# Kernel tuning notes

Measured on AMD Instinct MI355X. Metric: run time of the kernel, lower is better.

## Reference

```python
import jax, jax.numpy as jnp
import numpy as np

N = 100000       # nodes
E = 1200000      # edges (before self loops)
IN = 3
H = 64           # hidden
HNUM = 256       # number of direct virtual nodes
L = 2            # layers - 1 (hidden GATConvs and VN MLPs)
NEG_SLOPE = 0.2  # GATConv default


def setup_inputs() -> dict:
    key = jax.random.key(0)
    ks = jax.random.split(key, 20)
    s_in = 1.0 / np.sqrt(IN)
    s_h = 1.0 / np.sqrt(H)
    inp = dict(
        x=jax.random.normal(ks[0], (N, IN), dtype=jnp.float32),
        edge_index=jax.random.randint(ks[1], (2, E), 0, N, dtype=jnp.int32),
        h_blocks=jax.random.randint(ks[2], (N,), 0, HNUM, dtype=jnp.int32),
        h_levels=jax.random.randint(ks[3], (N,), 0, 4, dtype=jnp.int32),
        h_num=HNUM,
        # initial GATConv(IN -> H)
        w_in=jax.random.normal(ks[4], (IN, H), dtype=jnp.float32) * s_in,
        a_src_in=jax.random.normal(ks[5], (H,), dtype=jnp.float32) * s_h,
        a_dst_in=jax.random.normal(ks[6], (H,), dtype=jnp.float32) * s_h,
        b_in=jnp.zeros((H,), dtype=jnp.float32),
        # L hidden GATConv(H -> H) layers, stacked
        w_l=jax.random.normal(ks[7], (L, H, H), dtype=jnp.float32) * s_h,
        a_src_l=jax.random.normal(ks[8], (L, H), dtype=jnp.float32) * s_h,
        a_dst_l=jax.random.normal(ks[9], (L, H), dtype=jnp.float32) * s_h,
        b_l=jnp.zeros((L, H), dtype=jnp.float32),
        # L virtual-node MLPs: Linear-ReLU-Linear-ReLU
        mlp_w1=jax.random.normal(ks[10], (L, H, H), dtype=jnp.float32) * s_h,
        mlp_b1=jnp.zeros((L, H), dtype=jnp.float32),
        mlp_w2=jax.random.normal(ks[11], (L, H, H), dtype=jnp.float32) * s_h,
        mlp_b2=jnp.zeros((L, H), dtype=jnp.float32),
        # virtualnode embedding, constant-initialized to 0 in original
        vn_emb=jnp.zeros((1, H), dtype=jnp.float32),
    )
    return inp


def _gat_conv(x, src, dst, n, W, a_src, a_dst, b):
    """PyG GATConv, heads=1, add_self_loops already in (src,dst)."""
    h = x @ W                                   # [n, H]
    alpha = jax.nn.leaky_relu((h @ a_src)[src] + (h @ a_dst)[dst], NEG_SLOPE)
    # softmax over incoming edges of each dst node (self-loops => nonempty)
    amax = jax.ops.segment_max(alpha, dst, num_segments=n)
    ex = jnp.exp(alpha - amax[dst])
    denom = jax.ops.segment_sum(ex, dst, num_segments=n)
    w = ex / denom[dst]                         # [E_total]
    out = jax.ops.segment_sum(w[:, None] * h[src], dst, num_segments=n)
    return out + b


def _mlp(v, w1, b1, w2, b2):
    return jax.nn.relu(jax.nn.relu(v @ w1 + b1) @ w2 + b2)


def reference(x, edge_index, h_blocks, h_levels, h_num,
              w_in, a_src_in, a_dst_in, b_in,
              w_l, a_src_l, a_dst_l, b_l,
              mlp_w1, mlp_b1, mlp_w2, mlp_b2, vn_emb):
    n = x.shape[0]
    loops = jnp.arange(n, dtype=edge_index.dtype)
    src = jnp.concatenate([edge_index[0], loops])
    dst = jnp.concatenate([edge_index[1], loops])

    out = _gat_conv(x, src, dst, n, w_in, a_src_in, a_dst_in, b_in)
    vn_direct = jnp.broadcast_to(vn_emb, (h_num, vn_emb.shape[1]))  # zeros init
    vn_root = vn_emb                                                # [1, H]

    for l in range(L):
        out = out + vn_direct[h_blocks]
        out = _gat_conv(out, src, dst, n, w_l[l], a_src_l[l], a_dst_l[l], b_l[l])
        vn_direct = jax.ops.segment_sum(out, h_blocks, num_segments=h_num) + vn_direct
        vn_direct = vn_direct + vn_root
        vn_root = jnp.sum(vn_direct, axis=0, keepdims=True) + vn_root
        # original applies ALL vn MLPs each layer (faithful reproduction)
        for m in range(L):
            vn_direct = _mlp(vn_direct, mlp_w1[m], mlp_b1[m], mlp_w2[m], mlp_b2[m])
            vn_root = _mlp(vn_root, mlp_w1[m], mlp_b1[m], mlp_w2[m], mlp_b2[m])
    return out
```

## Files before the change

### kernel.cpp

```cpp
#include <hip/hip_runtime.h>


typedef __attribute__((ext_vector_type(8))) short short8;
typedef __attribute__((ext_vector_type(4))) float f32x4;

__device__ __forceinline__ unsigned short f2bf(float x){
    unsigned u = __float_as_uint(x);
    unsigned r = (u + 0x7fffu + ((u >> 16) & 1u)) >> 16;
    return (unsigned short)r;
}
__device__ __forceinline__ float bf2f(unsigned short b){
    return __uint_as_float(((unsigned)b) << 16);
}

#define BSHIFT 9
#define CHUNK 4096
#define NSLICE 8

__device__ __forceinline__ int incl_scan256(int v, int* sums4){
    int lane = threadIdx.x & 63, w = threadIdx.x >> 6;
    int x = v;
    #pragma unroll
    for (int o = 1; o < 64; o <<= 1){ int t = __shfl_up(x, o, 64); if (lane >= o) x += t; }
    __syncthreads();
    if (lane == 63) sums4[w] = x;
    __syncthreads();
    for (int j = 0; j < w; ++j) x += sums4[j];
    return x;
}

__global__ __launch_bounds__(256) void k_count(const int* __restrict__ dst, int E, int NB,
                                               int* __restrict__ bucketCount,
                                               const int* __restrict__ hb, int N,
                                               int* __restrict__ hbBins){
    __shared__ int cnt[256], cnt2[256];
    cnt[threadIdx.x] = 0; cnt2[threadIdx.x] = 0;
    __syncthreads();
    int base = blockIdx.x*CHUNK;
    int lim = min(base + CHUNK, E);
    for (int i = base + threadIdx.x; i < lim; i += 256)
        atomicAdd(&cnt[dst[i] >> BSHIFT], 1);
    int limN = min(base + CHUNK, N);
    for (int i = base + threadIdx.x; i < limN; i += 256)
        atomicAdd(&cnt2[hb[i]], 1);
    __syncthreads();
    if (threadIdx.x < NB && cnt[threadIdx.x])
        atomicAdd(&bucketCount[threadIdx.x], cnt[threadIdx.x]);
    if (cnt2[threadIdx.x])
        atomicAdd(&hbBins[threadIdx.x], cnt2[threadIdx.x]);
}

__global__ __launch_bounds__(256) void k_scan_all(const int* __restrict__ bucketCount,
                                                  int NB, int E, int N,
                                                  int* __restrict__ bucketOff,
                                                  int* __restrict__ bucketCur,
                                                  int* __restrict__ rowptr,
                                                  const int* __restrict__ hbBins,
                                                  int* __restrict__ binptr,
                                                  int* __restrict__ bincur){
    __shared__ int sums4[4];
    int tid = threadIdx.x;
    int v = (tid < NB) ? bucketCount[tid] : 0;
    int x = incl_scan256(v, sums4);
    if (tid < NB){ bucketOff[tid] = x - v; bucketCur[tid] = x - v; }
    if (tid == NB-1) bucketOff[NB] = x;
    if (tid == 0) rowptr[N] = E;
    int v2 = hbBins[tid];
    int x2 = incl_scan256(v2, sums4);
    binptr[tid] = x2 - v2;
    bincur[tid] = x2 - v2;
    if (tid == 255) binptr[256] = x2;
}

__global__ __launch_bounds__(256) void k_bucket_place(const int* __restrict__ src,
                                                      const int* __restrict__ dst, int E, int NB,
                                                      int* __restrict__ bucketCur,
                                                      int2* __restrict__ pairs){
    __shared__ int cnt[256], binStart[256], binCur[256], chunkBase[256];
    __shared__ int sums4[4];
    __shared__ int2 lp[CHUNK];
    int tid = threadIdx.x;
    cnt[tid] = 0; binCur[tid] = 0;
    __syncthreads();
    int base = blockIdx.x*CHUNK;
    int s[16], d[16];
    #pragma unroll
    for (int k = 0; k < 16; ++k){
        int i = base + k*256 + tid;
        if (i < E){ s[k] = src[i]; d[k] = dst[i]; atomicAdd(&cnt[d[k] >> BSHIFT], 1); }
        else d[k] = -1;
    }
    __syncthreads();
    int v = cnt[tid];
    int x = incl_scan256(v, sums4);
    binStart[tid] = x - v;
    __syncthreads();
    #pragma unroll
    for (int k = 0; k < 16; ++k){
        if (d[k] >= 0){
            int b = d[k] >> BSHIFT;
            int p = binStart[b] + atomicAdd(&binCur[b], 1);
            lp[p] = make_int2(s[k], d[k]);
        }
    }
    if (tid < NB){
        int c = cnt[tid];
        chunkBase[tid] = c ? atomicAdd(&bucketCur[tid], c) : 0;
    }
    __syncthreads();
    int total = min(CHUNK, E - base);
    for (int i = tid; i < total; i += 256){
        int2 p = lp[i];
        int b = p.y >> BSHIFT;
        pairs[chunkBase[b] + (i - binStart[b])] = p;
    }
}

__global__ __launch_bounds__(256) void k_hb_place(const int* __restrict__ hb, int N,
                                                  int* __restrict__ bincur,
                                                  int* __restrict__ nodes){
    __shared__ int cnt[256], binStart[256], binCur[256], chunkBase[256];
    __shared__ int sums4[4];
    __shared__ int lp[CHUNK];
    __shared__ unsigned char lb[CHUNK];
    int tid = threadIdx.x;
    cnt[tid] = 0; binCur[tid] = 0;
    __syncthreads();
    int base = blockIdx.x*CHUNK;
    int key[16];
    #pragma unroll
    for (int k = 0; k < 16; ++k){
        int i = base + k*256 + tid;
        key[k] = (i < N) ? hb[i] : -1;
        if (key[k] >= 0) atomicAdd(&cnt[key[k]], 1);
    }
    __syncthreads();
    int v = cnt[tid];
    int x = incl_scan256(v, sums4);
    binStart[tid] = x - v;
    __syncthreads();
    #pragma unroll
    for (int k = 0; k < 16; ++k){
        if (key[k] >= 0){
            int p = binStart[key[k]] + atomicAdd(&binCur[key[k]], 1);
            lp[p] = base + k*256 + tid;
            lb[p] = (unsigned char)key[k];
        }
    }
    if (cnt[tid]) chunkBase[tid] = atomicAdd(&bincur[tid], cnt[tid]);
    __syncthreads();
    int total = min(CHUNK, N - base);
    for (int i = tid; i < total; i += 256){
        int b = lb[i];
        nodes[chunkBase[b] + (i - binStart[b])] = lp[i];
    }
}

__global__ __launch_bounds__(256) void k_bucket_csr(const int2* __restrict__ pairs,
                                                    const int* __restrict__ bucketOff, int N,
                                                    int* __restrict__ rowptr,
                                                    int* __restrict__ colarr){
    __shared__ int deg[512], cur[512];
    __shared__ int sums4[4];
    __shared__ int tAs;
    int b = blockIdx.x, tid = threadIdx.x;
    int d0 = b << BSHIFT;
    int e0 = bucketOff[b], e1 = bucketOff[b+1];
    deg[tid] = 0; deg[256+tid] = 0;
    __syncthreads();
    for (int i = e0 + tid; i < e1; i += 256)
        atomicAdd(&deg[pairs[i].y - d0], 1);
    __syncthreads();
    int vA = deg[tid], vB = deg[256+tid];
    int xA = incl_scan256(vA, sums4);
    if (tid == 255) tAs = xA;
    int xB = incl_scan256(vB, sums4) + tAs;
    int exclA = xA - vA, exclB = xB - vB;
    cur[tid] = exclA; cur[256+tid] = exclB;
    int dA = d0 + tid, dB = d0 + 256 + tid;
    if (dA < N) rowptr[dA] = e0 + exclA;
    if (dB < N) rowptr[dB] = e0 + exclB;
    __syncthreads();
    for (int i = e0 + tid; i < e1; i += 256){
        int2 p = pairs[i];
        int pos = e0 + atomicAdd(&cur[p.y - d0], 1);
        colarr[pos] = p.x;
    }
}

__global__ __launch_bounds__(256) void k_transform_in(const float* __restrict__ x,
                                                      const float* __restrict__ W,
                                                      const float* __restrict__ a_src,
                                                      const float* __restrict__ a_dst,
                                                      unsigned short* __restrict__ hout,
                                                      float* __restrict__ ssrc,
                                                      float* __restrict__ sdst, int N){
    int wv = blockIdx.x*4 + (threadIdx.x >> 6);
    int lane = threadIdx.x & 63;
    if (wv >= N) return;
    float acc = 0.f;
    #pragma unroll
    for (int k = 0; k < 3; ++k)
        acc += x[wv*3 + k] * W[k*64 + lane];
    hout[(size_t)wv*64 + lane] = f2bf(acc);
    float v1 = acc * a_src[lane];
    float v2 = acc * a_dst[lane];
    #pragma unroll
    for (int o = 32; o; o >>= 1){ v1 += __shfl_xor(v1, o, 64); v2 += __shfl_xor(v2, o, 64); }
    if (lane == 0){ ssrc[wv] = v1; sdst[wv] = v2; }
}

#define LDW 72
__global__ __launch_bounds__(256) void k_transform_h_mfma(const float* __restrict__ feat,
                                                          const float* __restrict__ vn,
                                                          const float* __restrict__ vn_emb,
                                                          const int* __restrict__ hb,
                                                          const float* __restrict__ W,
                                                          const float* __restrict__ a_src,
                                                          const float* __restrict__ a_dst,
                                                          unsigned short* __restrict__ hout,
                                                          float* __restrict__ ssrc,
                                                          float* __restrict__ sdst, int N){
    __shared__ unsigned short WhT[64*LDW], WlT[64*LDW], Ah[64*LDW], Al[64*LDW];
    const int n0 = blockIdx.x * 64;

    for (int idx = threadIdx.x; idx < 4096; idx += 256){
        int n = idx >> 6, k = idx & 63;
        float w = W[k*64 + n];
        unsigned short hi = f2bf(w);
        WhT[n*LDW + k] = hi;
        WlT[n*LDW + k] = f2bf(w - bf2f(hi));
    }
    for (int t = threadIdx.x; t < 1024; t += 256){
        int row = t >> 4, c4 = t & 15;
        int node = n0 + row;
        float4 v = make_float4(0.f,0.f,0.f,0.f);
        if (node < N){
            v = ((const float4*)feat)[(size_t)node*16 + c4];
            float4 g = vn ? ((const float4*)vn)[(size_t)hb[node]*16 + c4]
                          : ((const float4*)vn_emb)[c4];
            v.x += g.x; v.y += g.y; v.z += g.z; v.w += g.w;
        }
        int base = row*LDW + c4*4;
        unsigned short h0 = f2bf(v.x), h1 = f2bf(v.y), h2 = f2bf(v.z), h3 = f2bf(v.w);
        Ah[base+0] = h0; Al[base+0] = f2bf(v.x - bf2f(h0));
        Ah[base+1] = h1; Al[base+1] = f2bf(v.y - bf2f(h1));
        Ah[base+2] = h2; Al[base+2] = f2bf(v.z - bf2f(h2));
        Ah[base+3] = h3; Al[base+3] = f2bf(v.w - bf2f(h3));
    }
    __syncthreads();

    int lane = threadIdx.x & 63;
    int wv   = threadIdx.x >> 6;
    int mrow = lane & 15, quad = lane >> 4;
    int m0 = wv * 16;

    f32x4 acc0 = {0,0,0,0}, acc1 = {0,0,0,0}, acc2 = {0,0,0,0}, acc3 = {0,0,0,0};
    #pragma unroll
    for (int k0 = 0; k0 < 64; k0 += 32){
        int kb = k0 + quad*8;
        short8 ah = *(const short8*)&Ah[(m0+mrow)*LDW + kb];
        short8 al = *(const short8*)&Al[(m0+mrow)*LDW + kb];
        short8 b0h = *(const short8*)&WhT[( 0+mrow)*LDW + kb];
        short8 b1h = *(const short8*)&WhT[(16+mrow)*LDW + kb];
        short8 b2h = *(const short8*)&WhT[(32+mrow)*LDW + kb];
        short8 b3h = *(const short8*)&WhT[(48+mrow)*LDW + kb];
        short8 b0l = *(const short8*)&WlT[( 0+mrow)*LDW + kb];
        short8 b1l = *(const short8*)&WlT[(16+mrow)*LDW + kb];
        short8 b2l = *(const short8*)&WlT[(32+mrow)*LDW + kb];
        short8 b3l = *(const short8*)&WlT[(48+mrow)*LDW + kb];
        acc0 = __builtin_amdgcn_mfma_f32_16x16x32_bf16(ah, b0h, acc0, 0, 0, 0);
        acc1 = __builtin_amdgcn_mfma_f32_16x16x32_bf16(ah, b1h, acc1, 0, 0, 0);
        acc2 = __builtin_amdgcn_mfma_f32_16x16x32_bf16(ah, b2h, acc2, 0, 0, 0);
        acc3 = __builtin_amdgcn_mfma_f32_16x16x32_bf16(ah, b3h, acc3, 0, 0, 0);
        acc0 = __builtin_amdgcn_mfma_f32_16x16x32_bf16(ah, b0l, acc0, 0, 0, 0);
        acc1 = __builtin_amdgcn_mfma_f32_16x16x32_bf16(ah, b1l, acc1, 0, 0, 0);
        acc2 = __builtin_amdgcn_mfma_f32_16x16x32_bf16(ah, b2l, acc2, 0, 0, 0);
        acc3 = __builtin_amdgcn_mfma_f32_16x16x32_bf16(ah, b3l, acc3, 0, 0, 0);
        acc0 = __builtin_amdgcn_mfma_f32_16x16x32_bf16(al, b0h, acc0, 0, 0, 0);
        acc1 = __builtin_amdgcn_mfma_f32_16x16x32_bf16(al, b1h, acc1, 0, 0, 0);
        acc2 = __builtin_amdgcn_mfma_f32_16x16x32_bf16(al, b2h, acc2, 0, 0, 0);
        acc3 = __builtin_amdgcn_mfma_f32_16x16x32_bf16(al, b3h, acc3, 0, 0, 0);
    }

    float as0 = a_src[mrow], as1 = a_src[16+mrow], as2 = a_src[32+mrow], as3 = a_src[48+mrow];
    float ad0 = a_dst[mrow], ad1 = a_dst[16+mrow], ad2 = a_dst[32+mrow], ad3 = a_dst[48+mrow];
    #pragma unroll
    for (int r = 0; r < 4; ++r){
        float p1 = acc0[r]*as0 + acc1[r]*as1 + acc2[r]*as2 + acc3[r]*as3;
        float p2 = acc0[r]*ad0 + acc1[r]*ad1 + acc2[r]*ad2 + acc3[r]*ad3;
        #pragma unroll
        for (int o = 8; o; o >>= 1){ p1 += __shfl_xor(p1, o, 64); p2 += __shfl_xor(p2, o, 64); }
        int node = n0 + m0 + quad*4 + r;
        if (mrow == 0 && node < N){ ssrc[node] = p1; sdst[node] = p2; }
    }
    #pragma unroll
    for (int r = 0; r < 4; ++r){
        int row = m0 + quad*4 + r;
        Ah[row*LDW + mrow     ] = f2bf(acc0[r]);
        Ah[row*LDW + mrow + 16] = f2bf(acc1[r]);
        Ah[row*LDW + mrow + 32] = f2bf(acc2[r]);
        Ah[row*LDW + mrow + 48] = f2bf(acc3[r]);
    }
    int r2 = lane >> 2, seg = lane & 3;
    int node = n0 + m0 + r2;
    if (node < N){
        short8 va = *(const short8*)&Ah[(m0+r2)*LDW + seg*16];
        short8 vb = *(const short8*)&Ah[(m0+r2)*LDW + seg*16 + 8];
        *(short8*)&hout[(size_t)node*64 + seg*16]     = va;
        *(short8*)&hout[(size_t)node*64 + seg*16 + 8] = vb;
    }
}

__global__ __launch_bounds__(256) void k_aggregate(const unsigned short* __restrict__ h,
                                                   const float* __restrict__ ssrc,
                                                   const float* __restrict__ sdst,
                                                   const int* __restrict__ rowptr,
                                                   const int* __restrict__ col,
                                                   const float* __restrict__ bias,
                                                   float* __restrict__ out, int N){
    __shared__ float2 swb[4][64];
    int wv = threadIdx.x >> 6;
    int lane = threadIdx.x & 63;
    int half = lane >> 5, lane32 = lane & 31;
    int d = blockIdx.x*8 + wv*2 + half;
    if (d >= N) return;
    int r8 = lane32 >> 3, c8 = lane32 & 7;
    float sd = sdst[d];
    float a0 = ssrc[d] + sd; a0 = (a0 < 0.f) ? 0.2f*a0 : a0;
    float dlocal = 0.f;
    float acc[8] = {0,0,0,0,0,0,0,0};
    if (r8 == 0){
        uint4 u = *(const uint4*)&h[(size_t)d*64 + c8*8];
        acc[0] = __uint_as_float(u.x << 16); acc[1] = __uint_as_float(u.x & 0xffff0000u);
        acc[2] = __uint_as_float(u.y << 16); acc[3] = __uint_as_float(u.y & 0xffff0000u);
        acc[4] = __uint_as_float(u.z << 16); acc[5] = __uint_as_float(u.z & 0xffff0000u);
        acc[6] = __uint_as_float(u.w << 16); acc[7] = __uint_as_float(u.w & 0xffff0000u);
    }
    int e0 = rowptr[d], e1 = rowptr[d+1];
    for (int base = e0; base < e1; base += 32){
        int ne = min(32, e1 - base);
        float w = 0.f; int s = 0;
        if (lane32 < ne){
            s = col[base + lane32];
            float a = ssrc[s] + sd;
            a = (a < 0.f) ? 0.2f*a : a;
            w = __expf(a - a0);
        }
        dlocal += w;
        swb[wv][lane] = make_float2(w, __int_as_float(s));
        int nj = (ne + 3) >> 2;
        for (int j = 0; j < nj; ++j){
            float2 p = swb[wv][half*32 + j*4 + r8];
            int sj = __float_as_int(p.y);
            uint4 u = *(const uint4*)&h[(size_t)sj*64 + c8*8];
            acc[0] += p.x * __uint_as_float(u.x << 16);
            acc[1] += p.x * __uint_as_float(u.x & 0xffff0000u);
            acc[2] += p.x * __uint_as_float(u.y << 16);
            acc[3] += p.x * __uint_as_float(u.y & 0xffff0000u);
            acc[4] += p.x * __uint_as_float(u.z << 16);
            acc[5] += p.x * __uint_as_float(u.z & 0xffff0000u);
            acc[6] += p.x * __uint_as_float(u.w << 16);
            acc[7] += p.x * __uint_as_float(u.w & 0xffff0000u);
        }
    }
    #pragma unroll
    for (int o = 16; o; o >>= 1) dlocal += __shfl_xor(dlocal, o, 64);
    float denom = 1.0f + dlocal;
    #pragma unroll
    for (int o = 8; o <= 16; o <<= 1){
        #pragma unroll
        for (int k = 0; k < 8; ++k) acc[k] += __shfl_xor(acc[k], o, 64);
    }
    if (r8 == 0){
        float inv = 1.0f/denom;
        float4 b4a = ((const float4*)bias)[c8*2];
        float4 b4b = ((const float4*)bias)[c8*2 + 1];
        float4 o1 = make_float4(acc[0]*inv + b4a.x, acc[1]*inv + b4a.y,
                                acc[2]*inv + b4a.z, acc[3]*inv + b4a.w);
        float4 o2 = make_float4(acc[4]*inv + b4b.x, acc[5]*inv + b4b.y,
                                acc[6]*inv + b4b.z, acc[7]*inv + b4b.w);
        ((float4*)out)[(size_t)d*16 + c8*2    ] = o1;
        ((float4*)out)[(size_t)d*16 + c8*2 + 1] = o2;
    }
}

__global__ __launch_bounds__(256) void k_vn_segsum2(const float* __restrict__ outA,
                                                    const int* __restrict__ nodes,
                                                    const int* __restrict__ binptr,
                                                    float* __restrict__ vseg){
    __shared__ float part[4][64];
    int b = blockIdx.x >> 3, s = blockIdx.x & (NSLICE-1);
    int wv = threadIdx.x >> 6, lane = threadIdx.x & 63;
    int i0 = binptr[b], i1 = binptr[b+1];
    int len = i1 - i0;
    int lo = i0 + (len*s)/NSLICE;
    int hi = i0 + (len*(s+1))/NSLICE;
    float acc = 0.f;
    for (int i = lo + wv; i < hi; i += 4){
        int n = nodes[i];
        acc += outA[(size_t)n*64 + lane];
    }
    part[wv][lane] = acc;
    __syncthreads();
    if (threadIdx.x < 64)
        vseg[(size_t)blockIdx.x*64 + lane] =
            part[0][lane] + part[1][lane] + part[2][lane] + part[3][lane];
}

__global__ __launch_bounds__(256) void k_vn_combine(const float* __restrict__ vseg,
                                                    const float* __restrict__ vd_old,
                                                    const float* __restrict__ root_old,
                                                    const float* __restrict__ vn_emb,
                                                    float* __restrict__ vw){
    __shared__ float part[4][64];
    int wv = threadIdx.x >> 6, lane = threadIdx.x & 63;
    float rold = root_old ? root_old[lane] : vn_emb[lane];
    float emb  = vn_emb[lane];
    float csum = 0.f;
    for (int b = wv*64; b < wv*64 + 64; ++b){
        float v = 0.f;
        #pragma unroll
        for (int s = 0; s < NSLICE; ++s)
            v += vseg[(size_t)(b*NSLICE + s)*64 + lane];
        v += (vd_old ? vd_old[b*64 + lane] : emb) + rold;
        vw[b*64 + lane] = v;
        csum += v;
    }
    part[wv][lane] = csum;
    __syncthreads();
    if (threadIdx.x < 64)
        vw[256*64 + lane] = part[0][lane] + part[1][lane] + part[2][lane] + part[3][lane] + rold;
}

__global__ __launch_bounds__(256) void k_vn_mlp(const float* __restrict__ mlp_w1,
                                                const float* __restrict__ mlp_b1,
                                                const float* __restrict__ mlp_w2,
                                                const float* __restrict__ mlp_b2,
                                                int L, float* __restrict__ vw){
    __shared__ float Wl[64*64];
    int wv = blockIdx.x*4 + (threadIdx.x >> 6);
    int lane = threadIdx.x & 63;
    bool valid = (wv < 257);
    float iv = valid ? vw[wv*64 + lane] : 0.f;
    for (int m = 0; m < L; ++m){
        #pragma unroll
        for (int half = 0; half < 2; ++half){
            const float* W    = (half ? mlp_w2 : mlp_w1) + (size_t)m*4096;
            const float* bias = (half ? mlp_b2 : mlp_b1) + (size_t)m*64;
            __syncthreads();
            for (int i = threadIdx.x; i < 4096; i += 256) Wl[i] = W[i];
            __syncthreads();
            float acc = bias[lane];
            #pragma unroll
            for (int k = 0; k < 64; ++k)
                acc += __shfl(iv, k, 64) * Wl[k*64 + lane];
            iv = fmaxf(acc, 0.f);
        }
    }
    if (valid) vw[wv*64 + lane] = iv;
}

extern "C" void kernel_launch(void* const* d_in, const int* in_sizes, int n_in,
                              void* d_out, int out_size, void* d_ws, size_t ws_size,
                              hipStream_t stream) {
    const int N = in_sizes[0] / 3;
    const int E = in_sizes[1] / 2;
    const int L = in_sizes[9] / (64*64);
    const int NB = (N + (1<<BSHIFT) - 1) >> BSHIFT;

    const float* x        = (const float*)d_in[0];
    const int*   edge     = (const int*)d_in[1];
    const int*   srcp     = edge;
    const int*   dstp     = edge + E;
    const int*   hb       = (const int*)d_in[2];
    const float* w_in     = (const float*)d_in[5];
    const float* a_src_in = (const float*)d_in[6];
    const float* a_dst_in = (const float*)d_in[7];
    const float* b_in     = (const float*)d_in[8];
    const float* w_l      = (const float*)d_in[9];
    const float* a_src_l  = (const float*)d_in[10];
    const float* a_dst_l  = (const float*)d_in[11];
    const float* b_l      = (const float*)d_in[12];
    const float* mlp_w1   = (const float*)d_in[13];
    const float* mlp_b1   = (const float*)d_in[14];
    const float* mlp_w2   = (const float*)d_in[15];
    const float* mlp_b2   = (const float*)d_in[16];
    const float* vn_emb   = (const float*)d_in[17];
    float*       out      = (float*)d_out;

    char* ws = (char*)d_ws;
    size_t off = 0;
    auto carve = [&](size_t bytes) -> char* {
        char* p = ws + off;
        off = (off + bytes + 255) & ~(size_t)255;
        return p;
    };
    unsigned short* h = (unsigned short*)carve((size_t)N*64*2);
    float* outA   = (float*)carve((size_t)N*64*4);
    float* ssrc   = (float*)carve((size_t)N*4);
    float* sdst   = (float*)carve((size_t)N*4);
    int*   rowptr = (int*)carve((size_t)(N+1)*4);
    char*  zstart = ws + off;
    int*   bucketCount = (int*)carve(256*4);
    int*   hbBins = (int*)carve(256*4);
    size_t zbytes = (size_t)((ws + off) - zstart);
    int*   bucketOff = (int*)carve(257*4);
    int*   bucketCur = (int*)carve(256*4);
    int*   binptr = (int*)carve(257*4);
    int*   bincur = (int*)carve(256*4);
    int*   colarr = (int*)carve((size_t)E*4);
    int*   nodes  = (int*)carve((size_t)N*4);
    float* vseg   = (float*)carve((size_t)256*NSLICE*64*4);
    float* vw     = (float*)carve((size_t)257*64*4);
    if (off > ws_size) return;
    int2* pairs = (int2*)h;

    hipMemsetAsync(zstart, 0, zbytes, stream);
    const int nchunkE = (E + CHUNK - 1) / CHUNK;
    const int nchunkN = (N + CHUNK - 1) / CHUNK;
    k_count       <<<nchunkE, 256, 0, stream>>>(dstp, E, NB, bucketCount, hb, N, hbBins);
    k_scan_all    <<<1, 256, 0, stream>>>(bucketCount, NB, E, N, bucketOff, bucketCur, rowptr,
                                          hbBins, binptr, bincur);
    k_bucket_place<<<nchunkE, 256, 0, stream>>>(srcp, dstp, E, NB, bucketCur, pairs);
    k_bucket_csr  <<<NB, 256, 0, stream>>>(pairs, bucketOff, N, rowptr, colarr);
    k_hb_place    <<<nchunkN, 256, 0, stream>>>(hb, N, bincur, nodes);

    const int nwb = (N + 3) / 4;
    const int nab = (N + 7) / 8;
    const int nmb = (N + 63) / 64;

    k_transform_in<<<nwb, 256, 0, stream>>>(x, w_in, a_src_in, a_dst_in, h, ssrc, sdst, N);
    k_aggregate<<<nab, 256, 0, stream>>>(h, ssrc, sdst, rowptr, colarr, b_in, outA, N);

    for (int l = 0; l < L; ++l){
        const float* vnp = (l == 0) ? nullptr : vw;
        k_transform_h_mfma<<<nmb, 256, 0, stream>>>(outA, vnp, vn_emb, hb,
                                                    w_l + (size_t)l*4096,
                                                    a_src_l + (size_t)l*64,
                                                    a_dst_l + (size_t)l*64,
                                                    h, ssrc, sdst, N);
        const bool last = (l == L-1);
        float* dst_buf = last ? out : outA;
        k_aggregate<<<nab, 256, 0, stream>>>(h, ssrc, sdst, rowptr, colarr,
                                             b_l + (size_t)l*64, dst_buf, N);
        if (!last){
            const float* vdo = (l == 0) ? nullptr : vw;
            const float* ro  = (l == 0) ? nullptr : (vw + 256*64);
            k_vn_segsum2<<<256*NSLICE, 256, 0, stream>>>(outA, nodes, binptr, vseg);
            k_vn_combine<<<1, 256, 0, stream>>>(vseg, vdo, ro, vn_emb, vw);
            k_vn_mlp<<<(257+3)/4, 256, 0, stream>>>(mlp_w1, mlp_b1, mlp_w2, mlp_b2, L, vw);
        }
    }
}
```

Before: 373.1 us.

## Use 16-lane groups per destination with batched gathers; parallelize VN combine

The aggregation kernel now gives each destination node 16 lanes instead of 32, handles 16 edges per iteration, and issues eight independent bf16 row gathers before accumulating. This is meant to raise memory-level parallelism and cut idle lanes on low-degree nodes, where the average degree is about 13. The cost is unconditional loads of 8 slots per iteration and more register pressure. The virtual-node combine moves from a single block to 64 blocks, computing the root column sum through atomics into a zeroed buffer that the MLP kernel reads.

```diff
diff --git a/kernel.cpp b/kernel.cpp
--- a/kernel.cpp
+++ b/kernel.cpp
@@ -322,15 +322,15 @@
     __shared__ float2 swb[4][64];
     int wv = threadIdx.x >> 6;
     int lane = threadIdx.x & 63;
-    int half = lane >> 5, lane32 = lane & 31;
-    int d = blockIdx.x*8 + wv*2 + half;
+    int grp = lane >> 4, lane16 = lane & 15;
+    int d = blockIdx.x*16 + wv*4 + grp;
     if (d >= N) return;
-    int r8 = lane32 >> 3, c8 = lane32 & 7;
+    int r2 = lane16 >> 3, c8 = lane16 & 7;
     float sd = sdst[d];
     float a0 = ssrc[d] + sd; a0 = (a0 < 0.f) ? 0.2f*a0 : a0;
     float dlocal = 0.f;
     float acc[8] = {0,0,0,0,0,0,0,0};
-    if (r8 == 0){
+    if (r2 == 0){
         uint4 u = *(const uint4*)&h[(size_t)d*64 + c8*8];
         acc[0] = __uint_as_float(u.x << 16); acc[1] = __uint_as_float(u.x & 0xffff0000u);
         acc[2] = __uint_as_float(u.y << 16); acc[3] = __uint_as_float(u.y & 0xffff0000u);
@@ -338,41 +338,44 @@
         acc[6] = __uint_as_float(u.w << 16); acc[7] = __uint_as_float(u.w & 0xffff0000u);
     }
     int e0 = rowptr[d], e1 = rowptr[d+1];
-    for (int base = e0; base < e1; base += 32){
-        int ne = min(32, e1 - base);
+    for (int base = e0; base < e1; base += 16){
+        int ne = min(16, e1 - base);
         float w = 0.f; int s = 0;
-        if (lane32 < ne){
-            s = col[base + lane32];
+        if (lane16 < ne){
+            s = col[base + lane16];
             float a = ssrc[s] + sd;
             a = (a < 0.f) ? 0.2f*a : a;
             w = __expf(a - a0);
         }
         dlocal += w;
         swb[wv][lane] = make_float2(w, __int_as_float(s));
-        int nj = (ne + 3) >> 2;
-        for (int j = 0; j < nj; ++j){
-            float2 p = swb[wv][half*32 + j*4 + r8];
-            int sj = __float_as_int(p.y);
-            uint4 u = *(const uint4*)&h[(size_t)sj*64 + c8*8];
-            acc[0] += p.x * __uint_as_float(u.x << 16);
-            acc[1] += p.x * __uint_as_float(u.x & 0xffff0000u);
-            acc[2] += p.x * __uint_as_float(u.y << 16);
-            acc[3] += p.x * __uint_as_float(u.y & 0xffff0000u);
-            acc[4] += p.x * __uint_as_float(u.z << 16);
-            acc[5] += p.x * __uint_as_float(u.z & 0xffff0000u);
-            acc[6] += p.x * __uint_as_float(u.w << 16);
-            acc[7] += p.x * __uint_as_float(u.w & 0xffff0000u);
-        }
-    }
-    #pragma unroll
-    for (int o = 16; o; o >>= 1) dlocal += __shfl_xor(dlocal, o, 64);
+        float2 p[8];
+        #pragma unroll
+        for (int j = 0; j < 8; ++j) p[j] = swb[wv][grp*16 + j*2 + r2];
+        uint4 u[8];
+        #pragma unroll
+        for (int j = 0; j < 8; ++j){
+            int sj = __float_as_int(p[j].y);
+            u[j] = *(const uint4*)&h[(size_t)sj*64 + c8*8];
+        }
+        #pragma unroll
+        for (int j = 0; j < 8; ++j){
+            acc[0] += p[j].x * __uint_as_float(u[j].x << 16);
+            acc[1] += p[j].x * __uint_as_float(u[j].x & 0xffff0000u);
+            acc[2] += p[j].x * __uint_as_float(u[j].y << 16);
+            acc[3] += p[j].x * __uint_as_float(u[j].y & 0xffff0000u);
+            acc[4] += p[j].x * __uint_as_float(u[j].z << 16);
+            acc[5] += p[j].x * __uint_as_float(u[j].z & 0xffff0000u);
+            acc[6] += p[j].x * __uint_as_float(u[j].w << 16);
+            acc[7] += p[j].x * __uint_as_float(u[j].w & 0xffff0000u);
+        }
+    }
+    #pragma unroll
+    for (int o = 8; o; o >>= 1) dlocal += __shfl_xor(dlocal, o, 64);
     float denom = 1.0f + dlocal;
     #pragma unroll
-    for (int o = 8; o <= 16; o <<= 1){
-        #pragma unroll
-        for (int k = 0; k < 8; ++k) acc[k] += __shfl_xor(acc[k], o, 64);
-    }
-    if (r8 == 0){
+    for (int k = 0; k < 8; ++k) acc[k] += __shfl_xor(acc[k], 8, 64);
+    if (r2 == 0){
         float inv = 1.0f/denom;
         float4 b4a = ((const float4*)bias)[c8*2];
         float4 b4b = ((const float4*)bias)[c8*2 + 1];
@@ -412,28 +415,24 @@
                                                     const float* __restrict__ vd_old,
                                                     const float* __restrict__ root_old,
                                                     const float* __restrict__ vn_emb,
-                                                    float* __restrict__ vw){
-    __shared__ float part[4][64];
+                                                    float* __restrict__ vw,
+                                                    float* __restrict__ colsum){
     int wv = threadIdx.x >> 6, lane = threadIdx.x & 63;
+    int b = blockIdx.x*4 + wv;
     float rold = root_old ? root_old[lane] : vn_emb[lane];
-    float emb  = vn_emb[lane];
-    float csum = 0.f;
-    for (int b = wv*64; b < wv*64 + 64; ++b){
-        float v = 0.f;
-        #pragma unroll
-        for (int s = 0; s < NSLICE; ++s)
-            v += vseg[(size_t)(b*NSLICE + s)*64 + lane];
-        v += (vd_old ? vd_old[b*64 + lane] : emb) + rold;
-        vw[b*64 + lane] = v;
-        csum += v;
-    }
-    part[wv][lane] = csum;
-    __syncthreads();
-    if (threadIdx.x < 64)
-        vw[256*64 + lane] = part[0][lane] + part[1][lane] + part[2][lane] + part[3][lane] + rold;
-}
-
-__global__ __launch_bounds__(256) void k_vn_mlp(const float* __restrict__ mlp_w1,
+    float v = 0.f;
+    #pragma unroll
+    for (int s = 0; s < NSLICE; ++s)
+        v += vseg[(size_t)(b*NSLICE + s)*64 + lane];
+    v += (vd_old ? vd_old[b*64 + lane] : vn_emb[lane]) + rold;
+    vw[b*64 + lane] = v;
+    atomicAdd(&colsum[lane], v);
+}
+
+__global__ __launch_bounds__(256) void k_vn_mlp(const float* __restrict__ colsum,
+                                                const float* __restrict__ root_old,
+                                                const float* __restrict__ vn_emb,
+                                                const float* __restrict__ mlp_w1,
                                                 const float* __restrict__ mlp_b1,
                                                 const float* __restrict__ mlp_w2,
                                                 const float* __restrict__ mlp_b2,
@@ -442,7 +441,15 @@
     int wv = blockIdx.x*4 + (threadIdx.x >> 6);
     int lane = threadIdx.x & 63;
     bool valid = (wv < 257);
-    float iv = valid ? vw[wv*64 + lane] : 0.f;
+    float iv = 0.f;
+    if (valid){
+        if (wv == 256){
+            float rold = root_old ? root_old[lane] : vn_emb[lane];
+            iv = colsum[lane] + rold;
+        } else {
+            iv = vw[wv*64 + lane];
+        }
+    }
     for (int m = 0; m < L; ++m){
         #pragma unroll
         for (int half = 0; half < 2; ++half){
@@ -504,6 +511,7 @@
     char*  zstart = ws + off;
     int*   bucketCount = (int*)carve(256*4);
     int*   hbBins = (int*)carve(256*4);
+    float* colsum = (float*)carve(64*4);
     size_t zbytes = (size_t)((ws + off) - zstart);
     int*   bucketOff = (int*)carve(257*4);
     int*   bucketCur = (int*)carve(256*4);
@@ -527,7 +535,7 @@
     k_hb_place    <<<nchunkN, 256, 0, stream>>>(hb, N, bincur, nodes);
 
     const int nwb = (N + 3) / 4;
-    const int nab = (N + 7) / 8;
+    const int nab = (N + 15) / 16;
     const int nmb = (N + 63) / 64;
 
     k_transform_in<<<nwb, 256, 0, stream>>>(x, w_in, a_src_in, a_dst_in, h, ssrc, sdst, N);
@@ -548,8 +556,9 @@
             const float* vdo = (l == 0) ? nullptr : vw;
             const float* ro  = (l == 0) ? nullptr : (vw + 256*64);
             k_vn_segsum2<<<256*NSLICE, 256, 0, stream>>>(outA, nodes, binptr, vseg);
-            k_vn_combine<<<1, 256, 0, stream>>>(vseg, vdo, ro, vn_emb, vw);
-            k_vn_mlp<<<(257+3)/4, 256, 0, stream>>>(mlp_w1, mlp_b1, mlp_w2, mlp_b2, L, vw);
-        }
-    }
-}
+            k_vn_combine<<<64, 256, 0, stream>>>(vseg, vdo, ro, vn_emb, vw, colsum);
+            k_vn_mlp<<<(257+3)/4, 256, 0, stream>>>(colsum, ro, vn_emb,
+                                                    mlp_w1, mlp_b1, mlp_w2, mlp_b2, L, vw);
+        }
+    }
+}
```

Measured after the change: 341.5 us. -8.5%, faster.
